# Kernel optimization log

Measured on AMD Instinct MI355X. Metric: run time of the kernel, lower is better.

The kernel has to match this reference:

```python
import jax, jax.numpy as jnp
import numpy as np

N_NODES = 100000
N_EDGES = 1600000
NFEAT = 128
NHID = 64


def setup_inputs() -> dict:
    key = jax.random.key(0)
    k1, k2, k3, k4 = jax.random.split(key, 4)
    x = jax.random.normal(k1, (N_NODES, NFEAT), dtype=jnp.float32)
    edge_index = jax.random.randint(k2, (2, N_EDGES), 0, N_NODES, dtype=jnp.int64)
    # Glorot-ish scaled weights
    W1 = jax.random.normal(k3, (NFEAT, NHID), dtype=jnp.float32) * (1.0 / np.sqrt(NFEAT))
    b1 = jnp.zeros((NHID,), dtype=jnp.float32)
    W2 = jax.random.normal(k4, (NHID, NFEAT), dtype=jnp.float32) * (1.0 / np.sqrt(NHID))
    b2 = jnp.zeros((NFEAT,), dtype=jnp.float32)
    return {"x": x, "edge_index": edge_index, "W1": W1, "b1": b1, "W2": W2, "b2": b2}


def _gcn_norm(edge_index, num_nodes):
    # PyG GCNConv default: add self-loops, symmetric normalization D^-1/2 A D^-1/2
    src, dst = edge_index[0], edge_index[1]
    loops = jnp.arange(num_nodes, dtype=src.dtype)
    src = jnp.concatenate([src, loops])
    dst = jnp.concatenate([dst, loops])
    ones = jnp.ones(src.shape[0], dtype=jnp.float32)
    deg = jax.ops.segment_sum(ones, dst, num_segments=num_nodes)  # in-degree incl. self-loop
    dinv = jax.lax.rsqrt(deg)  # deg >= 1 due to self-loops
    norm = dinv[src] * dinv[dst]  # [E + N]
    return src, dst, norm


def _gcn_conv(h, W, b, src, dst, norm, num_nodes):
    h = h @ W                                  # [N, d_out] transform first (d_out small)
    msg = norm[:, None] * h[src]               # gather over edges [E+N, d_out]
    out = jax.ops.segment_sum(msg, dst, num_segments=num_nodes)  # scatter-add
    return out + b


def reference(x, edge_index, W1, b1, W2, b2):
    num_nodes = x.shape[0]
    src, dst, norm = _gcn_norm(edge_index, num_nodes)
    h = jax.nn.relu(_gcn_conv(x, W1, b1, src, dst, norm, num_nodes))
    # dropout is identity in eval mode (deterministic reference baseline)
    out = _gcn_conv(h, W2, b2, src, dst, norm, num_nodes)
    return out
```

## Files before the change

### kernel.cpp

```cpp
#include <hip/hip_runtime.h>
#include <hip/hip_fp16.h>

#define NFEAT 128
#define NHID 64
#define MAXB 1024
#define BSHIFT 8
#define BNODES 256
#define PBLK 512
#define DBINS 512

typedef _Float16 f16x8 __attribute__((ext_vector_type(8)));
typedef float f32x4 __attribute__((ext_vector_type(4)));


__device__ __forceinline__ int edge_idx(const int* __restrict__ ei, int is64,
                                        long long E, long long e, int which) {
    long long pos = which ? (E + e) : e;
    return is64 ? ei[2 * pos] : ei[pos];
}

__device__ __forceinline__ void load8(const int* __restrict__ ei, int is64,
                                      long long E, long long e0, int which,
                                      int (&v)[8]) {
    if (is64) {
        const int* base = ei + 2 * (which ? E + e0 : e0);
        int4 a = *(const int4*)(base + 0);
        int4 b = *(const int4*)(base + 4);
        int4 c = *(const int4*)(base + 8);
        int4 d = *(const int4*)(base + 12);
        v[0] = a.x; v[1] = a.z; v[2] = b.x; v[3] = b.z;
        v[4] = c.x; v[5] = c.z; v[6] = d.x; v[7] = d.z;
    } else {
        const int* base = ei + (which ? E + e0 : e0);
        int4 a = *(const int4*)(base + 0);
        int4 b = *(const int4*)(base + 4);
        v[0] = a.x; v[1] = a.y; v[2] = a.z; v[3] = a.w;
        v[4] = b.x; v[5] = b.y; v[6] = b.z; v[7] = b.w;
    }
}

__device__ __forceinline__ int block_is64(const int* __restrict__ ei, int* smem) {
    if (threadIdx.x == 0) smem[0] = 0;
    __syncthreads();
    int acc = 0;
    for (int i = 1 + 2 * (int)threadIdx.x; i < 4096; i += 512)
        acc |= ei[i];
    atomicOr(&smem[0], acc);
    __syncthreads();
    int r = (smem[0] == 0) ? 1 : 0;
    __syncthreads();
    return r;
}

__global__ __launch_bounds__(256) void k_hist(const int* __restrict__ ei, long long E,
                                              long long perblk,
                                              int* __restrict__ blockhist, int NB) {
    __shared__ int smem[1024];
    int is64 = block_is64(ei, smem);
    int* hist = smem;
    for (int i = threadIdx.x; i < NB; i += 256) hist[i] = 0;
    __syncthreads();
    long long lo = (long long)blockIdx.x * perblk;
    long long hi = lo + perblk; if (hi > E) hi = E;
    if (lo < hi) {
        for (long long e0 = lo + (long long)threadIdx.x * 8; e0 + 8 <= hi; e0 += 256 * 8) {
            int d[8];
            load8(ei, is64, E, e0, 1, d);
#pragma unroll
            for (int j = 0; j < 8; ++j)
                atomicAdd(&hist[d[j] >> BSHIFT], 1);
        }
        long long tail = lo + ((hi - lo) & ~7LL);
        for (long long e = tail + threadIdx.x; e < hi; e += 256) {
            int d = edge_idx(ei, is64, E, e, 1);
            atomicAdd(&hist[d >> BSHIFT], 1);
        }
    }
    __syncthreads();
    int* bh = blockhist + (size_t)blockIdx.x * MAXB;
    for (int i = threadIdx.x; i < NB; i += 256) bh[i] = hist[i];
}

__global__ __launch_bounds__(256) void k_colscan(int* __restrict__ blockhist,
                                                 int* __restrict__ gbhist,
                                                 int* __restrict__ deghist, int NB) {
    __shared__ int s[256];
    int b = blockIdx.x;
    int t = threadIdx.x;
    if (b < NB) {
        int v0 = blockhist[(size_t)(2 * t) * MAXB + b];
        int v1 = blockhist[(size_t)(2 * t + 1) * MAXB + b];
        int sum = v0 + v1;
        s[t] = sum;
        __syncthreads();
        for (int d = 1; d < 256; d <<= 1) {
            int val = (t >= d) ? s[t - d] : 0;
            __syncthreads();
            s[t] += val;
            __syncthreads();
        }
        int run = s[t] - sum;
        blockhist[(size_t)(2 * t) * MAXB + b] = run;
        blockhist[(size_t)(2 * t + 1) * MAXB + b] = run + v0;
        if (t == 255) gbhist[b] = s[255];
    } else {
        int idx = (b - NB) * 256 + t;
        if (idx < DBINS) deghist[idx] = 0;
    }
}

__global__ __launch_bounds__(256) void k_bscan(const int* __restrict__ gbhist, int NB,
                                               int* __restrict__ boff,
                                               int* __restrict__ offN) {
    __shared__ int s[256];
    int t = threadIdx.x;
    int v[4]; int sum = 0;
#pragma unroll
    for (int j = 0; j < 4; ++j) {
        int i = t * 4 + j;
        v[j] = (i < NB) ? gbhist[i] : 0;
        sum += v[j];
    }
    s[t] = sum;
    __syncthreads();
    for (int d = 1; d < 256; d <<= 1) {
        int val = (t >= d) ? s[t - d] : 0;
        __syncthreads();
        s[t] += val;
        __syncthreads();
    }
    int run = s[t] - sum;
#pragma unroll
    for (int j = 0; j < 4; ++j) {
        int i = t * 4 + j;
        if (i <= NB) boff[i] = run;
        run += v[j];
    }
    if (t == 255) *offN = s[255];
}

__global__ __launch_bounds__(256) void k_partition(const int* __restrict__ ei, long long E,
                                                   long long perblk,
                                                   const int* __restrict__ boff,
                                                   const int* __restrict__ blockhist,
                                                   unsigned* __restrict__ staging, int NB) {
    __shared__ int smem[1024];
    int is64 = block_is64(ei, smem);
    int* cur = smem;
    const int* bh = blockhist + (size_t)blockIdx.x * MAXB;
    for (int i = threadIdx.x; i < NB; i += 256)
        cur[i] = boff[i] + bh[i];
    __syncthreads();
    long long lo = (long long)blockIdx.x * perblk;
    long long hi = lo + perblk; if (hi > E) hi = E;
    if (lo < hi) {
        for (long long e0 = lo + (long long)threadIdx.x * 8; e0 + 8 <= hi; e0 += 256 * 8) {
            int s[8], d[8];
            load8(ei, is64, E, e0, 0, s);
            load8(ei, is64, E, e0, 1, d);
#pragma unroll
            for (int j = 0; j < 8; ++j) {
                int pos = atomicAdd(&cur[d[j] >> BSHIFT], 1);
                staging[pos] = (unsigned)s[j] | ((unsigned)(d[j] & (BNODES - 1)) << 24);
            }
        }
        long long tail = lo + ((hi - lo) & ~7LL);
        for (long long e = tail + threadIdx.x; e < hi; e += 256) {
            int s = edge_idx(ei, is64, E, e, 0);
            int d = edge_idx(ei, is64, E, e, 1);
            int pos = atomicAdd(&cur[d >> BSHIFT], 1);
            staging[pos] = (unsigned)s | ((unsigned)(d & (BNODES - 1)) << 24);
        }
    }
}

__global__ __launch_bounds__(256) void k_bucket(const unsigned* __restrict__ staging,
                                                const int* __restrict__ boff,
                                                int N, int NB,
                                                int* __restrict__ off,
                                                int* __restrict__ esrc,
                                                float* __restrict__ dinv,
                                                int* __restrict__ deghist) {
    __shared__ int cnt_s[BNODES];
    __shared__ int scan_s[BNODES];
    __shared__ int dh[DBINS];
    int t = threadIdx.x;
    for (int b = blockIdx.x; b < NB; b += gridDim.x) {
        int base = b << BSHIFT;
        cnt_s[t] = 0;
        dh[t] = 0; dh[t + 256] = 0;
        __syncthreads();
        int lo = boff[b], hi = boff[b + 1];
        for (int e = lo + t; e < hi; e += 256)
            atomicAdd(&cnt_s[staging[e] >> 24], 1);
        __syncthreads();
        int v = cnt_s[t];
        scan_s[t] = v;
        __syncthreads();
        for (int d = 1; d < 256; d <<= 1) {
            int val = (t >= d) ? scan_s[t - d] : 0;
            __syncthreads();
            scan_s[t] += val;
            __syncthreads();
        }
        int excl = scan_s[t] - v;
        int node = base + t;
        if (node < N) {
            off[node] = lo + excl;
            dinv[node] = rsqrtf((float)v + 1.0f);
            atomicAdd(&dh[v < (DBINS - 1) ? v : (DBINS - 1)], 1);
        }
        __syncthreads();
        if (dh[t])       atomicAdd(&deghist[t], dh[t]);
        if (dh[t + 256]) atomicAdd(&deghist[t + 256], dh[t + 256]);
        cnt_s[t] = lo + excl;
        __syncthreads();
        for (int e = lo + t; e < hi; e += 256) {
            unsigned sd = staging[e];
            int pos = atomicAdd(&cnt_s[sd >> 24], 1);
            esrc[pos] = (int)(sd & 0xFFFFFFu);
        }
        __syncthreads();
    }
}

__global__ __launch_bounds__(256) void k_dscan(const int* __restrict__ deghist,
                                               int* __restrict__ dcur) {
    __shared__ int s[256];
    int t = threadIdx.x;
    int v0 = deghist[2 * t], v1 = deghist[2 * t + 1];
    int sum = v0 + v1;
    s[t] = sum;
    __syncthreads();
    for (int d = 1; d < 256; d <<= 1) {
        int val = (t >= d) ? s[t - d] : 0;
        __syncthreads();
        s[t] += val;
        __syncthreads();
    }
    int run = s[t] - sum;
    dcur[2 * t] = run;
    dcur[2 * t + 1] = run + v0;
}

__global__ __launch_bounds__(256) void k_dperm(const int* __restrict__ off,
                                               int* __restrict__ dcur,
                                               int* __restrict__ perm, int N) {
    __shared__ int cnt[DBINS];
    __shared__ int base[DBINS];
    int t = threadIdx.x;
    cnt[t] = 0; cnt[t + 256] = 0;
    __syncthreads();
    int n = blockIdx.x * 256 + t;
    int b = 0, myidx = 0;
    if (n < N) {
        int deg = off[n + 1] - off[n];
        b = deg < (DBINS - 1) ? deg : (DBINS - 1);
        myidx = atomicAdd(&cnt[b], 1);
    }
    __syncthreads();
    int c0 = cnt[t];       if (c0) base[t] = atomicAdd(&dcur[t], c0);
    int c1 = cnt[t + 256]; if (c1) base[t + 256] = atomicAdd(&dcur[t + 256], c1);
    __syncthreads();
    if (n < N) perm[base[b] + myidx] = n;
}

__device__ __forceinline__ int swz(int row, int byteoff) {
    return (row << 8) + (byteoff ^ ((row & 7) << 4));
}
__device__ __forceinline__ int swz64(int row, int byteoff) {
    return (row << 7) + (byteoff ^ ((row & 7) << 4));
}

__global__ __launch_bounds__(256) void k_gemm1(const float* __restrict__ x,
                                               const float* __restrict__ W1,
                                               const float* __restrict__ dinv,
                                               __half* __restrict__ xw1s, int N) {
    __shared__ __align__(16) __half xs[64 * NFEAT];
    __shared__ __align__(16) __half ws[NHID * NFEAT];
    int t = threadIdx.x;
    for (int i = t; i < NFEAT * NHID; i += 256) {
        int k = i >> 6, n = i & 63;
        *(__half*)((char*)ws + swz(n, k * 2)) = __float2half(W1[i]);
    }
    int row0 = blockIdx.x * 64;
    for (int i = t; i < 64 * 32; i += 256) {
        int r = i >> 5, c4 = i & 31;
        int row = row0 + r;
        float4 v = (row < N) ? ((const float4*)x)[(size_t)row * 32 + c4]
                             : make_float4(0.f, 0.f, 0.f, 0.f);
        __half2 h0 = __floats2half2_rn(v.x, v.y);
        __half2 h1 = __floats2half2_rn(v.z, v.w);
        uint2 p = make_uint2(*(unsigned*)&h0, *(unsigned*)&h1);
        *(uint2*)((char*)xs + swz(r, c4 * 8)) = p;
    }
    __syncthreads();
    int wave = t >> 6, lane = t & 63;
    int lr = lane & 15, g = lane >> 4;
    int xrow = wave * 16 + lr;
    f16x8 xb[4];
#pragma unroll
    for (int kc = 0; kc < 4; ++kc)
        xb[kc] = *(const f16x8*)((const char*)xs + swz(xrow, kc * 64 + g * 16));
    int row = row0 + xrow;
    float di = (row < N) ? dinv[row] : 0.f;
#pragma unroll
    for (int c = 0; c < 4; ++c) {
        f32x4 acc = {0.f, 0.f, 0.f, 0.f};
#pragma unroll
        for (int kc = 0; kc < 4; ++kc) {
            f16x8 a = *(const f16x8*)((const char*)ws + swz(c * 16 + lr, kc * 64 + g * 16));
            acc = __builtin_amdgcn_mfma_f32_16x16x32_f16(a, xb[kc], acc, 0, 0, 0);
        }
        if (row < N) {
            __half2 o0 = __floats2half2_rn(di * acc[0], di * acc[1]);
            __half2 o1 = __floats2half2_rn(di * acc[2], di * acc[3]);
            uint2 p = make_uint2(*(unsigned*)&o0, *(unsigned*)&o1);
            *(uint2*)&xw1s[(size_t)row * NHID + c * 16 + g * 4] = p;
        }
    }
}

__device__ __forceinline__ void addhalf8(float2 (&acc)[4], uint4 p) {
    const __half2* hh = (const __half2*)&p;
#pragma unroll
    for (int j = 0; j < 4; ++j) {
        float2 v = __half22float2(hh[j]);
        acc[j].x += v.x; acc[j].y += v.y;
    }
}

__device__ __forceinline__ void gather_group(const int* __restrict__ off,
                                             const int* __restrict__ esrc,
                                             const uint4* __restrict__ feat4,
                                             int d, int li, int lo, int hi,
                                             float2 (&acc)[4]) {
#pragma unroll
    for (int j = 0; j < 4; ++j) acc[j] = make_float2(0.f, 0.f);
    int idx = (lo + li < hi) ? esrc[lo + li] : 0;
    for (int e = lo; e < hi; e += 8) {
        int nrem = hi - e;
        int cur = idx;
        int ne = e + 8;
        idx = (ne + li < hi) ? esrc[ne + li] : 0;
        if (nrem >= 8) {
#pragma unroll
            for (int j = 0; j < 8; ++j) {
                int s = __shfl(cur, j, 8);
                addhalf8(acc, feat4[(size_t)s * 8 + li]);
            }
        } else {
            for (int j = 0; j < nrem; ++j) {
                int s = __shfl(cur, j, 8);
                addhalf8(acc, feat4[(size_t)s * 8 + li]);
            }
        }
    }
    addhalf8(acc, feat4[(size_t)d * 8 + li]);
}

__global__ __launch_bounds__(256) void k_agg1(const int* __restrict__ off,
                                              const int* __restrict__ esrc,
                                              const int* __restrict__ perm,
                                              const float* __restrict__ dinv,
                                              const uint4* __restrict__ xw1s4,
                                              const float* __restrict__ b1,
                                              uint4* __restrict__ h4, int N) {
    int t = threadIdx.x;
    int lane = t & 63, wave = t >> 6;
    int g = lane >> 3, li = lane & 7;
    int slot = blockIdx.x * 32 + wave * 8 + g;
    bool valid = slot < N;
    int d  = valid ? perm[slot] : 0;
    int lo = valid ? off[d] : 0;
    int hi = valid ? off[d + 1] : 0;
    float2 acc[4];
    gather_group(off, esrc, xw1s4, d, li, lo, hi, acc);
    float dd = dinv[d];
    float4 bA = ((const float4*)b1)[li * 2 + 0];
    float4 bB = ((const float4*)b1)[li * 2 + 1];
    float v0 = fmaxf(dd * acc[0].x + bA.x, 0.f);
    float v1 = fmaxf(dd * acc[0].y + bA.y, 0.f);
    float v2 = fmaxf(dd * acc[1].x + bA.z, 0.f);
    float v3 = fmaxf(dd * acc[1].y + bA.w, 0.f);
    float v4 = fmaxf(dd * acc[2].x + bB.x, 0.f);
    float v5 = fmaxf(dd * acc[2].y + bB.y, 0.f);
    float v6 = fmaxf(dd * acc[3].x + bB.z, 0.f);
    float v7 = fmaxf(dd * acc[3].y + bB.w, 0.f);
    __half2 o[4];
    o[0] = __floats2half2_rn(dd * v0, dd * v1);
    o[1] = __floats2half2_rn(dd * v2, dd * v3);
    o[2] = __floats2half2_rn(dd * v4, dd * v5);
    o[3] = __floats2half2_rn(dd * v6, dd * v7);
    if (valid) h4[(size_t)d * 8 + li] = *(const uint4*)o;
}

__global__ __launch_bounds__(256) void k_agg2(const int* __restrict__ off,
                                              const int* __restrict__ esrc,
                                              const int* __restrict__ perm,
                                              const float* __restrict__ dinv,
                                              const uint4* __restrict__ h4,
                                              uint4* __restrict__ a2h,
                                              uint4* __restrict__ a2l, int N) {
    int t = threadIdx.x;
    int lane = t & 63, wave = t >> 6;
    int g = lane >> 3, li = lane & 7;
    int slot = blockIdx.x * 32 + wave * 8 + g;
    bool valid = slot < N;
    int d  = valid ? perm[slot] : 0;
    int lo = valid ? off[d] : 0;
    int hi = valid ? off[d + 1] : 0;
    float2 acc[4];
    gather_group(off, esrc, h4, d, li, lo, hi, acc);
    float dd = dinv[d];
    float v[8] = {dd * acc[0].x, dd * acc[0].y, dd * acc[1].x, dd * acc[1].y,
                  dd * acc[2].x, dd * acc[2].y, dd * acc[3].x, dd * acc[3].y};
    __half hh[8], ll[8];
#pragma unroll
    for (int j = 0; j < 8; ++j) {
        hh[j] = __float2half(v[j]);
        ll[j] = __float2half(v[j] - __half2float(hh[j]));
    }
    uint4 ph, pl;
    __half2* hp = (__half2*)&ph;
    __half2* lp = (__half2*)&pl;
#pragma unroll
    for (int j = 0; j < 4; ++j) {
        hp[j] = __halves2half2(hh[2 * j], hh[2 * j + 1]);
        lp[j] = __halves2half2(ll[2 * j], ll[2 * j + 1]);
    }
    if (valid) {
        a2h[(size_t)d * 8 + li] = ph;
        a2l[(size_t)d * 8 + li] = pl;
    }
}

__global__ __launch_bounds__(256) void k_gemm2(const __half* __restrict__ a2h,
                                               const __half* __restrict__ a2l,
                                               const float* __restrict__ W2,
                                               const float* __restrict__ b2,
                                               float* __restrict__ out, int N) {
    __shared__ __align__(16) __half sB[NFEAT * NHID];
    __shared__ __align__(16) __half sH[64 * NHID];
    __shared__ __align__(16) __half sL[64 * NHID];
    int t = threadIdx.x;
    for (int i = t; i < NFEAT * NHID; i += 256) {
        int k = i >> 7, n = i & 127;
        *(__half*)((char*)sB + swz64(n, k * 2)) = __float2half(W2[i]);
    }
    int row0 = blockIdx.x * 64;
    for (int i = t; i < 64 * 8; i += 256) {
        int r = i >> 3, c16 = (i & 7) << 4;
        int row = row0 + r;
        uint4 vh = make_uint4(0, 0, 0, 0), vl = make_uint4(0, 0, 0, 0);
        if (row < N) {
            vh = *(const uint4*)((const char*)a2h + (size_t)row * 128 + c16);
            vl = *(const uint4*)((const char*)a2l + (size_t)row * 128 + c16);
        }
        *(uint4*)((char*)sH + swz64(r, c16)) = vh;
        *(uint4*)((char*)sL + swz64(r, c16)) = vl;
    }
    __syncthreads();
    int wave = t >> 6, lane = t & 63;
    int lr = lane & 15, g = lane >> 4;
    int xrow = wave * 16 + lr;
    f16x8 xh[2], xl[2];
#pragma unroll
    for (int kc = 0; kc < 2; ++kc) {
        xh[kc] = *(const f16x8*)((const char*)sH + swz64(xrow, kc * 64 + g * 16));
        xl[kc] = *(const f16x8*)((const char*)sL + swz64(xrow, kc * 64 + g * 16));
    }
    int row = row0 + xrow;
#pragma unroll
    for (int c = 0; c < 8; ++c) {
        f32x4 acc = {0.f, 0.f, 0.f, 0.f};
#pragma unroll
        for (int kc = 0; kc < 2; ++kc) {
            f16x8 a = *(const f16x8*)((const char*)sB + swz64(c * 16 + lr, kc * 64 + g * 16));
            acc = __builtin_amdgcn_mfma_f32_16x16x32_f16(a, xl[kc], acc, 0, 0, 0);
            acc = __builtin_amdgcn_mfma_f32_16x16x32_f16(a, xh[kc], acc, 0, 0, 0);
        }
        if (row < N) {
            float4 bb = *(const float4*)&b2[c * 16 + g * 4];
            float4 o = make_float4(acc[0] + bb.x, acc[1] + bb.y,
                                   acc[2] + bb.z, acc[3] + bb.w);
            *(float4*)&out[(size_t)row * NFEAT + c * 16 + g * 4] = o;
        }
    }
}

static inline char* align256(char* p) {
    return (char*)(((uintptr_t)p + 255) & ~(uintptr_t)255);
}

extern "C" void kernel_launch(void* const* d_in, const int* in_sizes, int n_in,
                              void* d_out, int out_size, void* d_ws, size_t ws_size,
                              hipStream_t stream) {
    const float* x  = (const float*)d_in[0];
    const int*   ei = (const int*)d_in[1];
    const float* W1 = (const float*)d_in[2];
    const float* b1 = (const float*)d_in[3];
    const float* W2 = (const float*)d_in[4];
    const float* b2 = (const float*)d_in[5];
    float* out = (float*)d_out;

    const int N = in_sizes[0] / NFEAT;
    const long long E = in_sizes[1] / 2;
    const int NB = (N + BNODES - 1) >> BSHIFT;

    char* w = (char*)d_ws;
    int*      gbhist    = (int*)w;
    int*      boff      = gbhist + MAXB;
    int*      deghist   = boff + MAXB + 1;
    int*      dcur      = deghist + DBINS;
    int*      blockhist = dcur + DBINS;
    float*    dinv      = (float*)(blockhist + (size_t)PBLK * MAXB);
    int*      off       = (int*)(dinv + N);
    int*      perm      = off + N + 1;
    char*     p         = align256((char*)(perm + N));
    unsigned* staging   = (unsigned*)p;
    p = align256((char*)(staging + E));
    int*      esrc      = (int*)p;
    p = align256((char*)(esrc + E));
    __half*   xw1s      = (__half*)p;
    p = align256((char*)(xw1s + (size_t)N * NHID));
    __half*   h         = (__half*)p;
    p = align256((char*)(h + (size_t)N * NHID));
    __half*   a2h       = (__half*)p;
    p = align256((char*)(a2h + (size_t)N * NHID));
    __half*   a2l       = (__half*)p;

    long long perblk = ((E + PBLK - 1) / PBLK + 7) & ~7LL;

    k_hist<<<PBLK, 256, 0, stream>>>(ei, E, perblk, blockhist, NB);
    k_colscan<<<NB + 2, 256, 0, stream>>>(blockhist, gbhist, deghist, NB);
    k_bscan<<<1, 256, 0, stream>>>(gbhist, NB, boff, off + N);
    k_partition<<<PBLK, 256, 0, stream>>>(ei, E, perblk, boff, blockhist, staging, NB);
    k_bucket<<<NB, 256, 0, stream>>>(staging, boff, N, NB, off, esrc, deghist ? dinv : dinv, deghist);
    k_dscan<<<1, 256, 0, stream>>>(deghist, dcur);
    k_dperm<<<(N + 255) / 256, 256, 0, stream>>>(off, dcur, perm, N);

    k_gemm1<<<(N + 63) / 64, 256, 0, stream>>>(x, W1, dinv, xw1s, N);

    k_agg1<<<(N + 31) / 32, 256, 0, stream>>>(off, esrc, perm, dinv, (const uint4*)xw1s,
                                              b1, (uint4*)h, N);
    k_agg2<<<(N + 31) / 32, 256, 0, stream>>>(off, esrc, perm, dinv, (const uint4*)h,
                                              (uint4*)a2h, (uint4*)a2l, N);

    k_gemm2<<<(N + 63) / 64, 256, 0, stream>>>(a2h, a2l, W2, b2, out, N);
}
```

Measured before the change: 266.5 us.

## Build CSR with global per-node atomics instead of two-level bucket sort

Replaces the bucketed counting sort (block histograms, column scan, partition into staging, per-bucket local sort) with a direct CSR build: global atomic in-degree counts, a multi-block scan that also computes dinv and the degree histogram, then a scatter of source indices using per-node global atomic cursors. This removes the staging buffer pass and several kernels, cutting memory traffic and launches. The cost is heavy contention-free but scattered global atomics over 100k nodes and non-deterministic edge order within each row, which can change float summation order.

New measurement: 421.4 us. +58.1%, slower.

```diff
diff --git a/kernel.cpp b/kernel.cpp
--- a/kernel.cpp
+++ b/kernel.cpp
@@ -3,8 +3,6 @@
 
 #define NFEAT 128
 #define NHID 64
-#define MAXB 1024
-#define BSHIFT 8
 #define BNODES 256
 #define PBLK 512
 #define DBINS 512
@@ -52,14 +50,13 @@
     return r;
 }
 
-__global__ __launch_bounds__(256) void k_hist(const int* __restrict__ ei, long long E,
-                                              long long perblk,
-                                              int* __restrict__ blockhist, int NB) {
+__global__ __launch_bounds__(256) void k_deg(const int* __restrict__ ei, long long E,
+                                             long long perblk, int* __restrict__ deg,
+                                             int* __restrict__ deghist) {
     __shared__ int smem[1024];
     int is64 = block_is64(ei, smem);
-    int* hist = smem;
-    for (int i = threadIdx.x; i < NB; i += 256) hist[i] = 0;
-    __syncthreads();
+    if (blockIdx.x == 0)
+        for (int i = threadIdx.x; i < DBINS; i += 256) deghist[i] = 0;
     long long lo = (long long)blockIdx.x * perblk;
     long long hi = lo + perblk; if (hi > E) hi = E;
     if (lo < hi) {
@@ -68,58 +65,46 @@
             load8(ei, is64, E, e0, 1, d);
 #pragma unroll
             for (int j = 0; j < 8; ++j)
-                atomicAdd(&hist[d[j] >> BSHIFT], 1);
+                atomicAdd(&deg[d[j]], 1);
         }
         long long tail = lo + ((hi - lo) & ~7LL);
         for (long long e = tail + threadIdx.x; e < hi; e += 256) {
             int d = edge_idx(ei, is64, E, e, 1);
-            atomicAdd(&hist[d >> BSHIFT], 1);
-        }
-    }
-    __syncthreads();
-    int* bh = blockhist + (size_t)blockIdx.x * MAXB;
-    for (int i = threadIdx.x; i < NB; i += 256) bh[i] = hist[i];
-}
-
-__global__ __launch_bounds__(256) void k_colscan(int* __restrict__ blockhist,
-                                                 int* __restrict__ gbhist,
-                                                 int* __restrict__ deghist, int NB) {
+            atomicAdd(&deg[d], 1);
+        }
+    }
+}
+
+__global__ __launch_bounds__(256) void k_scan1(const int* __restrict__ deg, int N,
+                                               int* __restrict__ off,
+                                               float* __restrict__ dinv,
+                                               int* __restrict__ psum,
+                                               int* __restrict__ deghist) {
     __shared__ int s[256];
-    int b = blockIdx.x;
-    int t = threadIdx.x;
-    if (b < NB) {
-        int v0 = blockhist[(size_t)(2 * t) * MAXB + b];
-        int v1 = blockhist[(size_t)(2 * t + 1) * MAXB + b];
-        int sum = v0 + v1;
-        s[t] = sum;
-        __syncthreads();
-        for (int d = 1; d < 256; d <<= 1) {
-            int val = (t >= d) ? s[t - d] : 0;
-            __syncthreads();
-            s[t] += val;
-            __syncthreads();
-        }
-        int run = s[t] - sum;
-        blockhist[(size_t)(2 * t) * MAXB + b] = run;
-        blockhist[(size_t)(2 * t + 1) * MAXB + b] = run + v0;
-        if (t == 255) gbhist[b] = s[255];
+    __shared__ int dh[DBINS];
+    int t = threadIdx.x;
+    int n0 = blockIdx.x * 1024;
+    dh[t] = 0; dh[t + 256] = 0;
+    __syncthreads();
+    int v[4]; int sum = 0;
+    if (n0 + 1024 <= N) {
+        int4 dv = ((const int4*)deg)[(n0 >> 2) + t];
+        v[0] = dv.x; v[1] = dv.y; v[2] = dv.z; v[3] = dv.w;
     } else {
-        int idx = (b - NB) * 256 + t;
-        if (idx < DBINS) deghist[idx] = 0;
-    }
-}
-
-__global__ __launch_bounds__(256) void k_bscan(const int* __restrict__ gbhist, int NB,
-                                               int* __restrict__ boff,
-                                               int* __restrict__ offN) {
-    __shared__ int s[256];
-    int t = threadIdx.x;
-    int v[4]; int sum = 0;
+#pragma unroll
+        for (int j = 0; j < 4; ++j) {
+            int n = n0 + t * 4 + j;
+            v[j] = (n < N) ? deg[n] : 0;
+        }
+    }
 #pragma unroll
     for (int j = 0; j < 4; ++j) {
-        int i = t * 4 + j;
-        v[j] = (i < NB) ? gbhist[i] : 0;
+        int n = n0 + t * 4 + j;
         sum += v[j];
+        if (n < N) {
+            dinv[n] = rsqrtf((float)v[j] + 1.0f);
+            atomicAdd(&dh[v[j] < (DBINS - 1) ? v[j] : (DBINS - 1)], 1);
+        }
     }
     s[t] = sum;
     __syncthreads();
@@ -132,25 +117,93 @@
     int run = s[t] - sum;
 #pragma unroll
     for (int j = 0; j < 4; ++j) {
-        int i = t * 4 + j;
-        if (i <= NB) boff[i] = run;
+        int n = n0 + t * 4 + j;
+        if (n < N) off[n] = run;
         run += v[j];
     }
-    if (t == 255) *offN = s[255];
-}
-
-__global__ __launch_bounds__(256) void k_partition(const int* __restrict__ ei, long long E,
-                                                   long long perblk,
-                                                   const int* __restrict__ boff,
-                                                   const int* __restrict__ blockhist,
-                                                   unsigned* __restrict__ staging, int NB) {
+    if (t == 255) psum[blockIdx.x] = s[255];
+    __syncthreads();
+    if (dh[t])       atomicAdd(&deghist[t], dh[t]);
+    if (dh[t + 256]) atomicAdd(&deghist[t + 256], dh[t + 256]);
+}
+
+__global__ __launch_bounds__(256) void k_scan2(int* __restrict__ psum, int nsb,
+                                               const int* __restrict__ deghist,
+                                               int* __restrict__ dcur,
+                                               int* __restrict__ offN, int E32) {
+    __shared__ int s[256];
+    int t = threadIdx.x;
+    int v = (t < nsb) ? psum[t] : 0;
+    s[t] = v;
+    __syncthreads();
+    for (int d = 1; d < 256; d <<= 1) {
+        int val = (t >= d) ? s[t - d] : 0;
+        __syncthreads();
+        s[t] += val;
+        __syncthreads();
+    }
+    if (t < nsb) psum[t] = s[t] - v;
+    __syncthreads();
+    int v0 = deghist[2 * t], v1 = deghist[2 * t + 1];
+    int sum = v0 + v1;
+    s[t] = sum;
+    __syncthreads();
+    for (int d = 1; d < 256; d <<= 1) {
+        int val = (t >= d) ? s[t - d] : 0;
+        __syncthreads();
+        s[t] += val;
+        __syncthreads();
+    }
+    int run = s[t] - sum;
+    dcur[2 * t] = run;
+    dcur[2 * t + 1] = run + v0;
+    if (t == 0) *offN = E32;
+}
+
+__global__ __launch_bounds__(256) void k_scan3(int* __restrict__ off,
+                                               int* __restrict__ cur,
+                                               const int* __restrict__ psum,
+                                               const int* __restrict__ deg,
+                                               int* __restrict__ dcur,
+                                               int* __restrict__ perm, int N) {
+    __shared__ int cnt[DBINS];
+    __shared__ int base[DBINS];
+    int t = threadIdx.x;
+    int n0 = blockIdx.x * 1024;
+    int pfx = psum[blockIdx.x];
+    cnt[t] = 0; cnt[t + 256] = 0;
+    __syncthreads();
+    int b_[4], idx_[4];
+#pragma unroll
+    for (int j = 0; j < 4; ++j) {
+        int n = n0 + t * 4 + j;
+        b_[j] = 0; idx_[j] = 0;
+        if (n < N) {
+            int o = off[n] + pfx;
+            off[n] = o;
+            cur[n] = o;
+            int dg = deg[n];
+            int b = dg < (DBINS - 1) ? dg : (DBINS - 1);
+            b_[j] = b;
+            idx_[j] = atomicAdd(&cnt[b], 1);
+        }
+    }
+    __syncthreads();
+    int c0 = cnt[t];       if (c0) base[t] = atomicAdd(&dcur[t], c0);
+    int c1 = cnt[t + 256]; if (c1) base[t + 256] = atomicAdd(&dcur[t + 256], c1);
+    __syncthreads();
+#pragma unroll
+    for (int j = 0; j < 4; ++j) {
+        int n = n0 + t * 4 + j;
+        if (n < N) perm[base[b_[j]] + idx_[j]] = n;
+    }
+}
+
+__global__ __launch_bounds__(256) void k_scatter(const int* __restrict__ ei, long long E,
+                                                 long long perblk, int* __restrict__ cur,
+                                                 int* __restrict__ esrc) {
     __shared__ int smem[1024];
     int is64 = block_is64(ei, smem);
-    int* cur = smem;
-    const int* bh = blockhist + (size_t)blockIdx.x * MAXB;
-    for (int i = threadIdx.x; i < NB; i += 256)
-        cur[i] = boff[i] + bh[i];
-    __syncthreads();
     long long lo = (long long)blockIdx.x * perblk;
     long long hi = lo + perblk; if (hi > E) hi = E;
     if (lo < hi) {
@@ -160,109 +213,18 @@
             load8(ei, is64, E, e0, 1, d);
 #pragma unroll
             for (int j = 0; j < 8; ++j) {
-                int pos = atomicAdd(&cur[d[j] >> BSHIFT], 1);
-                staging[pos] = (unsigned)s[j] | ((unsigned)(d[j] & (BNODES - 1)) << 24);
+                int pos = atomicAdd(&cur[d[j]], 1);
+                esrc[pos] = s[j];
             }
         }
         long long tail = lo + ((hi - lo) & ~7LL);
         for (long long e = tail + threadIdx.x; e < hi; e += 256) {
             int s = edge_idx(ei, is64, E, e, 0);
             int d = edge_idx(ei, is64, E, e, 1);
-            int pos = atomicAdd(&cur[d >> BSHIFT], 1);
-            staging[pos] = (unsigned)s | ((unsigned)(d & (BNODES - 1)) << 24);
-        }
-    }
-}
-
-__global__ __launch_bounds__(256) void k_bucket(const unsigned* __restrict__ staging,
-                                                const int* __restrict__ boff,
-                                                int N, int NB,
-                                                int* __restrict__ off,
-                                                int* __restrict__ esrc,
-                                                float* __restrict__ dinv,
-                                                int* __restrict__ deghist) {
-    __shared__ int cnt_s[BNODES];
-    __shared__ int scan_s[BNODES];
-    __shared__ int dh[DBINS];
-    int t = threadIdx.x;
-    for (int b = blockIdx.x; b < NB; b += gridDim.x) {
-        int base = b << BSHIFT;
-        cnt_s[t] = 0;
-        dh[t] = 0; dh[t + 256] = 0;
-        __syncthreads();
-        int lo = boff[b], hi = boff[b + 1];
-        for (int e = lo + t; e < hi; e += 256)
-            atomicAdd(&cnt_s[staging[e] >> 24], 1);
-        __syncthreads();
-        int v = cnt_s[t];
-        scan_s[t] = v;
-        __syncthreads();
-        for (int d = 1; d < 256; d <<= 1) {
-            int val = (t >= d) ? scan_s[t - d] : 0;
-            __syncthreads();
-            scan_s[t] += val;
-            __syncthreads();
-        }
-        int excl = scan_s[t] - v;
-        int node = base + t;
-        if (node < N) {
-            off[node] = lo + excl;
-            dinv[node] = rsqrtf((float)v + 1.0f);
-            atomicAdd(&dh[v < (DBINS - 1) ? v : (DBINS - 1)], 1);
-        }
-        __syncthreads();
-        if (dh[t])       atomicAdd(&deghist[t], dh[t]);
-        if (dh[t + 256]) atomicAdd(&deghist[t + 256], dh[t + 256]);
-        cnt_s[t] = lo + excl;
-        __syncthreads();
-        for (int e = lo + t; e < hi; e += 256) {
-            unsigned sd = staging[e];
-            int pos = atomicAdd(&cnt_s[sd >> 24], 1);
-            esrc[pos] = (int)(sd & 0xFFFFFFu);
-        }
-        __syncthreads();
-    }
-}
-
-__global__ __launch_bounds__(256) void k_dscan(const int* __restrict__ deghist,
-                                               int* __restrict__ dcur) {
-    __shared__ int s[256];
-    int t = threadIdx.x;
-    int v0 = deghist[2 * t], v1 = deghist[2 * t + 1];
-    int sum = v0 + v1;
-    s[t] = sum;
-    __syncthreads();
-    for (int d = 1; d < 256; d <<= 1) {
-        int val = (t >= d) ? s[t - d] : 0;
-        __syncthreads();
-        s[t] += val;
-        __syncthreads();
-    }
-    int run = s[t] - sum;
-    dcur[2 * t] = run;
-    dcur[2 * t + 1] = run + v0;
-}
-
-__global__ __launch_bounds__(256) void k_dperm(const int* __restrict__ off,
-                                               int* __restrict__ dcur,
-                                               int* __restrict__ perm, int N) {
-    __shared__ int cnt[DBINS];
-    __shared__ int base[DBINS];
-    int t = threadIdx.x;
-    cnt[t] = 0; cnt[t + 256] = 0;
-    __syncthreads();
-    int n = blockIdx.x * 256 + t;
-    int b = 0, myidx = 0;
-    if (n < N) {
-        int deg = off[n + 1] - off[n];
-        b = deg < (DBINS - 1) ? deg : (DBINS - 1);
-        myidx = atomicAdd(&cnt[b], 1);
-    }
-    __syncthreads();
-    int c0 = cnt[t];       if (c0) base[t] = atomicAdd(&dcur[t], c0);
-    int c1 = cnt[t + 256]; if (c1) base[t + 256] = atomicAdd(&dcur[t + 256], c1);
-    __syncthreads();
-    if (n < N) perm[base[b] + myidx] = n;
+            int pos = atomicAdd(&cur[d], 1);
+            esrc[pos] = s;
+        }
+    }
 }
 
 __device__ __forceinline__ int swz(int row, int byteoff) {
@@ -506,39 +468,36 @@
 
     const int N = in_sizes[0] / NFEAT;
     const long long E = in_sizes[1] / 2;
-    const int NB = (N + BNODES - 1) >> BSHIFT;
+    const int NSB = (N + 1023) >> 10;
 
     char* w = (char*)d_ws;
-    int*      gbhist    = (int*)w;
-    int*      boff      = gbhist + MAXB;
-    int*      deghist   = boff + MAXB + 1;
-    int*      dcur      = deghist + DBINS;
-    int*      blockhist = dcur + DBINS;
-    float*    dinv      = (float*)(blockhist + (size_t)PBLK * MAXB);
-    int*      off       = (int*)(dinv + N);
-    int*      perm      = off + N + 1;
-    char*     p         = align256((char*)(perm + N));
-    unsigned* staging   = (unsigned*)p;
-    p = align256((char*)(staging + E));
-    int*      esrc      = (int*)p;
+    int*      deg     = (int*)w;
+    int*      off     = deg + N;
+    int*      cur     = off + N + 1;
+    int*      perm    = cur + N;
+    float*    dinv    = (float*)(perm + N);
+    int*      psum    = (int*)(dinv + N);
+    int*      deghist = psum + 256;
+    int*      dcur    = deghist + DBINS;
+    char*     p       = align256((char*)(dcur + DBINS));
+    int*      esrc    = (int*)p;
     p = align256((char*)(esrc + E));
-    __half*   xw1s      = (__half*)p;
+    __half*   xw1s    = (__half*)p;
     p = align256((char*)(xw1s + (size_t)N * NHID));
-    __half*   h         = (__half*)p;
+    __half*   h       = (__half*)p;
     p = align256((char*)(h + (size_t)N * NHID));
-    __half*   a2h       = (__half*)p;
+    __half*   a2h     = (__half*)p;
     p = align256((char*)(a2h + (size_t)N * NHID));
-    __half*   a2l       = (__half*)p;
+    __half*   a2l     = (__half*)p;
 
     long long perblk = ((E + PBLK - 1) / PBLK + 7) & ~7LL;
 
-    k_hist<<<PBLK, 256, 0, stream>>>(ei, E, perblk, blockhist, NB);
-    k_colscan<<<NB + 2, 256, 0, stream>>>(blockhist, gbhist, deghist, NB);
-    k_bscan<<<1, 256, 0, stream>>>(gbhist, NB, boff, off + N);
-    k_partition<<<PBLK, 256, 0, stream>>>(ei, E, perblk, boff, blockhist, staging, NB);
-    k_bucket<<<NB, 256, 0, stream>>>(staging, boff, N, NB, off, esrc, deghist ? dinv : dinv, deghist);
-    k_dscan<<<1, 256, 0, stream>>>(deghist, dcur);
-    k_dperm<<<(N + 255) / 256, 256, 0, stream>>>(off, dcur, perm, N);
+    hipMemsetAsync(deg, 0, (size_t)N * sizeof(int), stream);
+    k_deg<<<PBLK, 256, 0, stream>>>(ei, E, perblk, deg, deghist);
+    k_scan1<<<NSB, 256, 0, stream>>>(deg, N, off, dinv, psum, deghist);
+    k_scan2<<<1, 256, 0, stream>>>(psum, NSB, deghist, dcur, off + N, (int)E);
+    k_scan3<<<NSB, 256, 0, stream>>>(off, cur, psum, deg, dcur, perm, N);
+    k_scatter<<<PBLK, 256, 0, stream>>>(ei, E, perblk, cur, esrc);
 
     k_gemm1<<<(N + 63) / 64, 256, 0, stream>>>(x, W1, dinv, xw1s, N);
 
```
